# Kernel optimization log

Hardware: AMD Instinct MI355X
Metric: run time of the kernel (lower is better)

Reference implementation:

```python
import jax, jax.numpy as jnp
import numpy as np
from jax import lax

D_MODEL = 1024
D_INNER = 2 * D_MODEL          # expand=2
D_STATE = 16
D_CONV = 4
DT_RANK = 64                   # ceil(1024/16)
DT_MIN = 0.001
DT_MAX = 0.1
BATCH = 4
SEQ = 2048


def setup_inputs() -> dict:
    key = jax.random.key(0)
    ks = jax.random.split(key, 8)
    s = lambda fan_in: 1.0 / np.sqrt(fan_in)
    x = jax.random.normal(ks[0], (BATCH, SEQ, D_MODEL), dtype=jnp.float32)
    # Linear weights stored as (in, out) so y = x @ W
    W_in = jax.random.uniform(ks[1], (D_MODEL, 2 * D_INNER), jnp.float32, -s(D_MODEL), s(D_MODEL))
    conv_w = jax.random.uniform(ks[2], (D_INNER, 1, D_CONV), jnp.float32, -s(D_CONV), s(D_CONV))
    conv_b = jax.random.uniform(ks[3], (D_INNER,), jnp.float32, -s(D_CONV), s(D_CONV))
    W_x = jax.random.uniform(ks[4], (D_INNER, DT_RANK + 2 * D_STATE), jnp.float32, -s(D_INNER), s(D_INNER))
    W_dt = jax.random.uniform(ks[5], (DT_RANK, D_INNER), jnp.float32, -s(DT_RANK), s(DT_RANK))
    b_dt = jax.random.uniform(ks[6], (D_INNER,), jnp.float32, -s(DT_RANK), s(DT_RANK))
    # A = arange(1..d_state) repeated over d_inner; store log(A)
    A_log = jnp.log(jnp.broadcast_to(jnp.arange(1, D_STATE + 1, dtype=jnp.float32), (D_INNER, D_STATE)))
    D_param = jnp.ones((D_INNER,), dtype=jnp.float32)
    W_out = jax.random.uniform(ks[7], (D_INNER, D_MODEL), jnp.float32, -s(D_INNER), s(D_INNER))
    return {"x": x, "W_in": W_in, "conv_w": conv_w, "conv_b": conv_b,
            "W_x": W_x, "W_dt": W_dt, "b_dt": b_dt, "A_log": A_log,
            "D_param": D_param, "W_out": W_out}


def reference(x, W_in, conv_w, conv_b, W_x, W_dt, b_dt, A_log, D_param, W_out):
    # in_proj + split
    xz = x @ W_in                                   # (B, S, 2*d_inner)
    x_branch, z_branch = jnp.split(xz, 2, axis=-1)  # each (B, S, d_inner)

    # causal depthwise conv1d (torch pads d_conv-1 both sides then slices [:seq])
    xc = jnp.pad(x_branch.transpose(0, 2, 1), ((0, 0), (0, 0), (D_CONV - 1, 0)))
    xc = lax.conv_general_dilated(xc, conv_w, (1,), 'VALID',
                                  dimension_numbers=('NCH', 'OIH', 'NCH'),
                                  feature_group_count=D_INNER)
    xc = xc + conv_b[None, :, None]
    x_conv = jax.nn.silu(xc.transpose(0, 2, 1))     # (B, S, d_inner)

    # input-dependent dt, B, C
    x_dbl = x_conv @ W_x                            # (B, S, dt_rank + 2*d_state)
    dt_low = x_dbl[..., :DT_RANK]
    Bm = x_dbl[..., DT_RANK:DT_RANK + D_STATE]      # (B, S, d_state)
    Cm = x_dbl[..., DT_RANK + D_STATE:]             # (B, S, d_state)
    dt = jax.nn.sigmoid(dt_low @ W_dt + b_dt) * (DT_MAX - DT_MIN) + DT_MIN
    dt = jnp.maximum(dt, 1e-4)                      # (B, S, d_inner)

    A = -jnp.exp(A_log)                             # (d_inner, d_state)

    # selective scan over time (n_substeps = 1)
    def step(h, inp):
        dt_t, B_t, C_t, x_t = inp                   # (B,di), (B,ds), (B,ds), (B,di)
        dA = jnp.exp(dt_t[:, :, None] * A[None])    # (B, di, ds)
        h = dA * h + (dt_t * x_t)[:, :, None] * B_t[:, None, :]
        y_t = jnp.sum(h * C_t[:, None, :], axis=-1) # (B, di)
        return h, y_t

    h0 = jnp.zeros((x.shape[0], D_INNER, D_STATE), dtype=x.dtype)
    _, ys = lax.scan(step, h0,
                     (dt.swapaxes(0, 1), Bm.swapaxes(0, 1),
                      Cm.swapaxes(0, 1), x_conv.swapaxes(0, 1)))
    y = ys.swapaxes(0, 1)                           # (B, S, d_inner)

    y = y + x_conv * D_param
    y = y * jax.nn.silu(z_branch)
    return y @ W_out                                # (B, S, d_model)
```

## Files before the change

kernel.cpp:

```cpp
#include <hip/hip_runtime.h>

typedef unsigned short u16;
typedef unsigned int u32;
typedef __attribute__((ext_vector_type(8))) short short8;
typedef __attribute__((ext_vector_type(4))) short short4v;
typedef __attribute__((ext_vector_type(2))) short short2v;
typedef __attribute__((ext_vector_type(4))) float f32x4;

#define NBATCH 4
#define NSEQ   2048
#define DMODEL 1024
#define DINNER 2048
#define DSTATE 16
#define DTRANK 64
#define ROWS   (NBATCH*NSEQ)
#define NCH    64
#define CLEN   32

__device__ __forceinline__ float b2f(u16 u){ union{u32 i; float f;} v; v.i=((u32)u)<<16; return v.f; }
__device__ __forceinline__ u16 f2b(float f){ union{float f; u32 i;} v; v.f=f; u32 i=v.i; return (u16)((i + 0x7FFFu + ((i>>16)&1u))>>16); }
__device__ __forceinline__ float sigmoidf_(float x){ return 1.0f/(1.0f+__expf(-x)); }

__device__ __forceinline__ void pow16(float e1, float (&pw)[16]){
  float p2 = e1*e1, p4 = p2*p2, p8 = p4*p4;
  pw[0]=e1;        pw[1]=p2;        pw[2]=e1*p2;     pw[3]=p4;
  pw[4]=e1*p4;     pw[5]=p2*p4;     pw[6]=pw[2]*p4;  pw[7]=p8;
  pw[8]=e1*p8;     pw[9]=p2*p8;     pw[10]=pw[2]*p8; pw[11]=p4*p8;
  pw[12]=pw[4]*p8; pw[13]=pw[5]*p8; pw[14]=pw[6]*p8; pw[15]=p8*p8;
}

__global__ __launch_bounds__(256) void prep(const u16* __restrict__ x,
    const u16* __restrict__ Win, const u16* __restrict__ convw,
    const u16* __restrict__ Wx, const u16* __restrict__ Wdt,
    const u16* __restrict__ Alog, const u16* __restrict__ Wout,
    const u16* __restrict__ v0, const u16* __restrict__ v1, const u16* __restrict__ v2,
    int* __restrict__ meta){
  __shared__ int vote;
  __shared__ int mxbits;
  const int tid = threadIdx.x;
  const u16* V[3] = {v0, v1, v2};

  const u16* ptrs[6] = {x, Win, convw, Wx, Wdt, Wout};
  const float bounds[6] = {8.f, 0.045f, 0.6f, 0.035f, 0.15f, 0.035f};
  const int slots[6] = {0, 1, 2, 4, 5, 9};
  for (int q = 0; q < 6; q++){
    if (tid == 0) vote = 1;
    __syncthreads();
    int bad = 0;
    for (int i = tid; i < 2048; i += 256){
      float v = fabsf(b2f(ptrs[q][i]));
      if (!(v <= bounds[q])) bad = 1;
    }
    if (bad) atomicAnd(&vote, 0);
    __syncthreads();
    if (tid == 0) meta[slots[q]] = vote;
    __syncthreads();
  }
  if (tid == 0){ u16 u = Alog[1]; meta[7] = (u == 0x3F31 || u == 0x3F32) ? 1 : 0; }

  int iD = -1, fD = 1;
  for (int k = 0; k < 3; k++){
    if (V[k][0] == 0x3F80 && V[k][1] == 0x3F80){ iD = k; fD = 1; }
    else if (V[k][0] == 0 && V[k][1] == 0x3F80 && V[k][2] == 0){ iD = k; fD = 0; }
  }
  if (iD < 0){ iD = 2; fD = 1; }
  int oo[2], no = 0;
  for (int k = 0; k < 3; k++) if (k != iD) oo[no++] = k;
  int fo[2]; float mo[2];
  for (int q = 0; q < 2; q++){
    if (tid == 0) vote = 1;
    __syncthreads();
    int bad = 0;
    for (int i = tid; i < 2048; i += 256){
      float v = fabsf(b2f(V[oo[q]][i]));
      if (!(v <= 0.6f)) bad = 1;
    }
    if (bad) atomicAnd(&vote, 0);
    __syncthreads();
    fo[q] = vote;
    if (tid == 0) mxbits = 0;
    __syncthreads();
    float m = 0.f;
    for (int i = tid; i < 2048; i += 256){
      float v = fabsf(fo[q] ? b2f(V[oo[q]][i]) : ((const float*)V[oo[q]])[i]);
      m = fmaxf(m, v);
    }
    atomicMax(&mxbits, __float_as_int(m));
    __syncthreads();
    mo[q] = __int_as_float(mxbits);
    __syncthreads();
  }
  if (tid == 0){
    int a = (mo[0] > 0.25f) ? 0 : 1;
    meta[10] = oo[a];     meta[3] = fo[a];
    meta[11] = oo[1-a];   meta[6] = fo[1-a];
    meta[12] = iD;        meta[8] = fD;
  }
}

__global__ __launch_bounds__(256) void cvt_bf16(const void* __restrict__ in,
                                                u16* __restrict__ out, long n,
                                                const int* __restrict__ meta, int slot){
  long i = (long)blockIdx.x*256 + threadIdx.x;
  if (i >= n) return;
  if (meta[slot]) out[i] = ((const u16*)in)[i];
  else            out[i] = f2b(((const float*)in)[i]);
}

__global__ __launch_bounds__(256) void cvt_x8(const void* __restrict__ in,
                                              u16* __restrict__ out,
                                              const int* __restrict__ meta){
  long i8 = ((long)blockIdx.x*256 + threadIdx.x)*8;
  if (meta[0]){
    *(short8*)(out + i8) = *(const short8*)((const u16*)in + i8);
  } else {
    const float* f = (const float*)in + i8;
    f32x4 a = *(const f32x4*)f;
    f32x4 b = *(const f32x4*)(f+4);
    short8 o;
    #pragma unroll
    for (int j=0;j<4;j++){ ((u16*)&o)[j] = f2b(a[j]); ((u16*)&o)[4+j] = f2b(b[j]); }
    *(short8*)(out + i8) = o;
  }
}

__global__ __launch_bounds__(256) void cvt_trio(const void* __restrict__ v0,
                                                const void* __restrict__ v1,
                                                const void* __restrict__ v2,
                                                const int* __restrict__ meta,
                                                u16* __restrict__ cbc,
                                                u16* __restrict__ bdtc,
                                                u16* __restrict__ dpc){
  int i = blockIdx.x*256 + threadIdx.x;
  int which = i >> 11, d = i & 2047;
  const void* V[3] = {v0, v1, v2};
  int src, fl; u16* dst;
  if (which == 0){ src = meta[10]; fl = meta[3]; dst = cbc; }
  else if (which == 1){ src = meta[11]; fl = meta[6]; dst = bdtc; }
  else { src = meta[12]; fl = meta[8]; dst = dpc; }
  dst[d] = fl ? ((const u16*)V[src])[d] : f2b(((const float*)V[src])[d]);
}

__global__ __launch_bounds__(256) void transpose_pad(const void* __restrict__ inv,
                                                     u16* __restrict__ out,
                                                     int K, int N, int Nout,
                                                     const int* __restrict__ meta, int slot){
  __shared__ u16 t[32][33];
  const int f = meta[slot];
  const u16*   ib = (const u16*)inv;
  const float* iff = (const float*)inv;
  int k0 = blockIdx.x*32, n0 = blockIdx.y*32;
  int tx = threadIdx.x & 31, ty = threadIdx.x >> 5;
  #pragma unroll
  for (int i=0;i<32;i+=8){
    int k = k0+ty+i, n = n0+tx;
    u16 v = 0;
    if (k<K && n<N) v = f ? ib[(long)k*N+n] : f2b(iff[(long)k*N+n]);
    t[ty+i][tx] = v;
  }
  __syncthreads();
  #pragma unroll
  for (int i=0;i<32;i+=8){
    int n = n0+ty+i, k = k0+tx;
    if (n<Nout && k<K) out[(long)n*K+k] = t[tx][ty+i];
  }
}

template<int MODE>
__global__ __launch_bounds__(256) void gemm_bt(
    const u16* __restrict__ A, int lda,
    const u16* __restrict__ Bt, int K,
    u16* __restrict__ C0, u16* __restrict__ C1, int ldc,
    const u16* __restrict__ bias, float* __restrict__ Cf)
{
  __shared__ u16 sa[128*64];
  __shared__ u16 sb[128*64];
  const int tid = threadIdx.x;
  const int lane = tid & 63;
  const int wave = tid >> 6;
  const int wm = (wave >> 1) * 64;
  const int wn = (wave & 1) * 64;
  const int lane15 = lane & 15;
  const int quad = lane >> 4;
  const long rowBase = (long)blockIdx.y * 128;
  const long colBase = (long)blockIdx.x * 128;

  int kbeg = 0, kend = K;
  if (MODE == 4){
    const int span = K >> 2;
    kbeg = blockIdx.z * span;
    kend = kbeg + span;
    Cf += (long)blockIdx.z * (8192L*128);
  }

  f32x4 acc[4][4];
  #pragma unroll
  for (int i=0;i<4;i++)
    #pragma unroll
    for (int j=0;j<4;j++)
      #pragma unroll
      for (int r=0;r<4;r++) acc[i][j][r]=0.0f;

  const int e  = tid*8;
  const int r0 = e >> 6;
  const int c0 = e & 63;

  for (int kb=kbeg; kb<kend; kb+=64) {
    #pragma unroll
    for (int i=0;i<4;i++){
      const u16* ga = A + (rowBase + r0 + i*32)*lda + kb + c0;
      __builtin_amdgcn_global_load_lds((const __attribute__((address_space(1))) void*)ga,
                                       (__attribute__((address_space(3))) void*)&sa[e + i*2048],
                                       16, 0, 0);
    }
    #pragma unroll
    for (int i=0;i<4;i++){
      const u16* gb = Bt + (colBase + r0 + i*32)*(long)K + kb + c0;
      __builtin_amdgcn_global_load_lds((const __attribute__((address_space(1))) void*)gb,
                                       (__attribute__((address_space(3))) void*)&sb[e + i*2048],
                                       16, 0, 0);
    }
    __syncthreads();
    #pragma unroll
    for (int ko=0; ko<2; ko++){
      const int kk = ko*32 + quad*8;
      short8 af[4], bfr[4];
      #pragma unroll
      for (int i=0;i<4;i++) af[i]  = *(const short8*)&sa[(wm + i*16 + lane15)*64 + kk];
      #pragma unroll
      for (int j=0;j<4;j++) bfr[j] = *(const short8*)&sb[(wn + j*16 + lane15)*64 + kk];
      #pragma unroll
      for (int i=0;i<4;i++)
        #pragma unroll
        for (int j=0;j<4;j++)
          acc[i][j] = __builtin_amdgcn_mfma_f32_16x16x32_bf16(af[i], bfr[j], acc[i][j], 0, 0, 0);
    }
    __syncthreads();
  }

  #pragma unroll
  for (int i=0;i<4;i++){
    #pragma unroll
    for (int j=0;j<4;j++){
      long row = rowBase + wm + i*16 + quad*4;
      long col = colBase + wn + j*16 + lane15;
      #pragma unroll
      for (int r=0;r<4;r++){
        float v = acc[i][j][r];
        long rr = row + r;
        if (MODE == 0) {
          C0[rr*ldc + col] = f2b(v);
        } else if (MODE == 2) {
          float t  = sigmoidf_(v + b2f(bias[col]));
          float dv = fmaxf(t*0.099f + 0.001f, 1e-4f);
          C0[rr*ldc + col] = f2b(dv);
        } else if (MODE == 4) {
          Cf[rr*ldc + col] = v;
        }
      }
    }
  }
}

__global__ __launch_bounds__(256) void reduce_xdbl(const float* __restrict__ P,
                                                   u16* __restrict__ out){
  const long i4 = ((long)blockIdx.x*256 + threadIdx.x)*4;
  f32x4 a = *(const f32x4*)(P + i4);
  f32x4 b = *(const f32x4*)(P + 1048576 + i4);
  f32x4 c = *(const f32x4*)(P + 2097152 + i4);
  f32x4 d = *(const f32x4*)(P + 3145728 + i4);
  short4v o;
  #pragma unroll
  for (int j=0;j<4;j++) ((u16*)&o)[j] = f2b(a[j]+b[j]+c[j]+d[j]);
  *(short4v*)(out + i4) = o;
}

template<int MODE>
__global__ __launch_bounds__(512, 2) void gemm256(
    const u16* __restrict__ A, int lda,
    const u16* __restrict__ Bt, int K,
    u16* __restrict__ C0, u16* __restrict__ C1, int ldc,
    float* __restrict__ Cf)
{
  __shared__ u16 sa[2*16384];
  __shared__ u16 sb[2*16384];
  const int tid  = threadIdx.x;
  const int lane = tid & 63;
  const int wm   = (tid >> 6) >> 2;
  const int wn   = (tid >> 6) & 3;
  const int lane15 = lane & 15;
  const int quad   = lane >> 4;

  const int nwg  = gridDim.x * gridDim.y;
  const int orig = blockIdx.y * gridDim.x + blockIdx.x;
  const int swz  = (orig & 7) * (nwg >> 3) + (orig >> 3);
  const int bx   = swz % gridDim.x;
  const int by   = swz / gridDim.x;
  const long rowBase = (long)by * 256;
  const long colBase = (long)bx * 256;

  const int xorv = (lane15 & 7) << 3;
  const int k0   = (quad*8) ^ xorv;
  const int k1   = (32 + quad*8) ^ xorv;
  const int aBase = (wm*128 + lane15) * 64;
  const int bBase = (wn*64  + lane15) * 64;

  const int scol = ((tid & 7) ^ ((tid >> 3) & 7)) << 3;
  const int arow = tid >> 3;
  const int bsub = ((tid >> 8) & 1)*64 + ((tid & 255) >> 3);
  const int bdst = (tid & 7) * 8;

  f32x4 acc[8][4];
  #pragma unroll
  for (int i=0;i<8;i++)
    #pragma unroll
    for (int j=0;j<4;j++)
      #pragma unroll
      for (int r=0;r<4;r++) acc[i][j][r]=0.0f;

  const int nt = K >> 6;

  auto stageA = [&](int buf, int rs, int kb){
    const u16* g = A + (rowBase + rs + arow)*(long)lda + kb + scol;
    __builtin_amdgcn_global_load_lds((const __attribute__((address_space(1))) void*)g,
        (__attribute__((address_space(3))) void*)&sa[buf*16384 + rs*64 + tid*8], 16, 0, 0);
  };
  auto stageB = [&](int buf, int cq, int part, int kb){
    const int row = part*128 + cq*32 + bsub;
    const u16* g = Bt + (colBase + row)*(long)K + kb + scol;
    __builtin_amdgcn_global_load_lds((const __attribute__((address_space(1))) void*)g,
        (__attribute__((address_space(3))) void*)&sb[buf*16384 + row*64 + bdst], 16, 0, 0);
  };

  stageA(0,   0, 0); stageA(0, 128, 0);
  stageB(0, 0, 0, 0); stageB(0, 0, 1, 0);
  stageA(0,  64, 0); stageA(0, 192, 0);
  stageB(0, 1, 0, 0); stageB(0, 1, 1, 0);
  asm volatile("s_waitcnt vmcnt(4)\n\ts_barrier" ::: "memory");

  for (int t = 0; t < nt; ++t){
    const int cur = t & 1, nb = cur ^ 1;
    const int kb2 = (t+1) << 6;
    const bool pf = (t+1 < nt);
    const u16* sA = &sa[cur*16384];
    const u16* sB = &sb[cur*16384];
    short8 a0[4][2], a1[4][2], b0[2][2], b1[2][2];

    #pragma unroll
    for (int i=0;i<4;i++){
      a0[i][0] = *(const short8*)&sA[aBase + i*1024 + k0];
      a0[i][1] = *(const short8*)&sA[aBase + i*1024 + k1];
    }
    #pragma unroll
    for (int j=0;j<2;j++){
      b0[j][0] = *(const short8*)&sB[bBase + j*1024 + k0];
      b0[j][1] = *(const short8*)&sB[bBase + j*1024 + k1];
    }
    if (pf){ stageA(nb, 0, kb2); stageA(nb, 128, kb2); }
    __builtin_amdgcn_s_setprio(1);
    #pragma unroll
    for (int s=0;s<2;s++)
      #pragma unroll
      for (int i=0;i<4;i++)
        #pragma unroll
        for (int j=0;j<2;j++)
          acc[i][j] = __builtin_amdgcn_mfma_f32_16x16x32_bf16(a0[i][s], b0[j][s], acc[i][j], 0, 0, 0);
    __builtin_amdgcn_s_setprio(0);
    asm volatile("s_waitcnt vmcnt(4)\n\ts_barrier" ::: "memory");

    #pragma unroll
    for (int i=0;i<4;i++){
      a1[i][0] = *(const short8*)&sA[aBase + 4096 + i*1024 + k0];
      a1[i][1] = *(const short8*)&sA[aBase + 4096 + i*1024 + k1];
    }
    if (pf){ stageB(nb, 0, 0, kb2); stageB(nb, 0, 1, kb2); }
    __builtin_amdgcn_s_setprio(1);
    #pragma unroll
    for (int s=0;s<2;s++)
      #pragma unroll
      for (int i=0;i<4;i++)
        #pragma unroll
        for (int j=0;j<2;j++)
          acc[4+i][j] = __builtin_amdgcn_mfma_f32_16x16x32_bf16(a1[i][s], b0[j][s], acc[4+i][j], 0, 0, 0);
    __builtin_amdgcn_s_setprio(0);
    asm volatile("s_waitcnt vmcnt(4)\n\ts_barrier" ::: "memory");

    #pragma unroll
    for (int j=0;j<2;j++){
      b1[j][0] = *(const short8*)&sB[bBase + 2048 + j*1024 + k0];
      b1[j][1] = *(const short8*)&sB[bBase + 2048 + j*1024 + k1];
    }
    if (pf){ stageA(nb, 64, kb2); stageA(nb, 192, kb2); }
    __builtin_amdgcn_s_setprio(1);
    #pragma unroll
    for (int s=0;s<2;s++)
      #pragma unroll
      for (int i=0;i<4;i++)
        #pragma unroll
        for (int j=0;j<2;j++)
          acc[i][2+j] = __builtin_amdgcn_mfma_f32_16x16x32_bf16(a0[i][s], b1[j][s], acc[i][2+j], 0, 0, 0);
    __builtin_amdgcn_s_setprio(0);
    asm volatile("s_barrier" ::: "memory");

    if (pf){ stageB(nb, 1, 0, kb2); stageB(nb, 1, 1, kb2); }
    __builtin_amdgcn_s_setprio(1);
    #pragma unroll
    for (int s=0;s<2;s++)
      #pragma unroll
      for (int i=0;i<4;i++)
        #pragma unroll
        for (int j=0;j<2;j++)
          acc[4+i][2+j] = __builtin_amdgcn_mfma_f32_16x16x32_bf16(a1[i][s], b1[j][s], acc[4+i][2+j], 0, 0, 0);
    __builtin_amdgcn_s_setprio(0);
    asm volatile("s_waitcnt vmcnt(4)\n\ts_barrier" ::: "memory");
  }

  #pragma unroll
  for (int i=0;i<8;i++){
    const long row = rowBase + wm*128 + i*16 + quad*4;
    #pragma unroll
    for (int j=0;j<4;j++){
      const long col = colBase + wn*64 + j*16 + lane15;
      #pragma unroll
      for (int r=0;r<4;r++){
        const float v = acc[i][j][r];
        const long rr = row + r;
        if (MODE == 1){
          if (col < 2048) C0[rr*2048 + col] = f2b(v);
          else            C1[rr*2048 + (col-2048)] = f2b(v);
        } else {
          Cf[rr*ldc + col] = v;
        }
      }
    }
  }
}

__global__ __launch_bounds__(512, 2) void gemm_out(
    const u16* __restrict__ A, int lda,
    const u16* __restrict__ Bt, int K,
    float* __restrict__ Cf, int ldc)
{
  __shared__ u16 sa[2*16384];
  __shared__ u16 sb[2*8192];
  const int tid  = threadIdx.x;
  const int lane = tid & 63;
  const int wm   = (tid >> 6) >> 2;
  const int wn   = (tid >> 6) & 3;
  const int lane15 = lane & 15;
  const int quad   = lane >> 4;

  const int nwg  = gridDim.x * gridDim.y;
  const int orig = blockIdx.y * gridDim.x + blockIdx.x;
  const int swz  = (orig & 7) * (nwg >> 3) + (orig >> 3);
  const int bx   = swz % gridDim.x;
  const int by   = swz / gridDim.x;
  const long rowBase = (long)by * 256;
  const long colBase = (long)bx * 128;

  const int xorv = (lane15 & 7) << 3;
  const int k0   = (quad*8) ^ xorv;
  const int k1   = (32 + quad*8) ^ xorv;
  const int aBase = (wm*128 + lane15) * 64;
  const int bBase = (wn*32  + lane15) * 64;

  const int scol = ((tid & 7) ^ ((tid >> 3) & 7)) << 3;
  const int arow = tid >> 3;

  f32x4 acc[8][2];
  #pragma unroll
  for (int i=0;i<8;i++)
    #pragma unroll
    for (int j=0;j<2;j++)
      #pragma unroll
      for (int r=0;r<4;r++) acc[i][j][r]=0.0f;

  const int nt = K >> 6;

  auto stageA = [&](int buf, int rs, int kb){
    const u16* g = A + (rowBase + rs + arow)*(long)lda + kb + scol;
    __builtin_amdgcn_global_load_lds((const __attribute__((address_space(1))) void*)g,
        (__attribute__((address_space(3))) void*)&sa[buf*16384 + rs*64 + tid*8], 16, 0, 0);
  };
  auto stageB = [&](int buf, int rs, int kb){
    const u16* g = Bt + (colBase + rs + arow)*(long)K + kb + scol;
    __builtin_amdgcn_global_load_lds((const __attribute__((address_space(1))) void*)g,
        (__attribute__((address_space(3))) void*)&sb[buf*8192 + rs*64 + tid*8], 16, 0, 0);
  };

  stageA(0,0,0); stageA(0,128,0); stageB(0,0,0); stageB(0,64,0);
  stageA(0,64,0); stageA(0,192,0);
  asm volatile("s_waitcnt vmcnt(0)\n\ts_barrier" ::: "memory");

  for (int t = 0; t < nt; ++t){
    const int cur = t & 1, nb = cur ^ 1;
    const int kb2 = (t+1) << 6;
    const bool pf = (t+1 < nt);
    const u16* sA = &sa[cur*16384];
    const u16* sB = &sb[cur*8192];
    short8 a0[4][2], a1[4][2], bf_[2][2];

    #pragma unroll
    for (int i=0;i<4;i++){
      a0[i][0] = *(const short8*)&sA[aBase + i*1024 + k0];
      a0[i][1] = *(const short8*)&sA[aBase + i*1024 + k1];
    }
    #pragma unroll
    for (int j=0;j<2;j++){
      bf_[j][0] = *(const short8*)&sB[bBase + j*1024 + k0];
      bf_[j][1] = *(const short8*)&sB[bBase + j*1024 + k1];
    }
    if (pf){ stageA(nb,0,kb2); stageA(nb,128,kb2); stageB(nb,0,kb2); stageB(nb,64,kb2); }
    __builtin_amdgcn_s_setprio(1);
    #pragma unroll
    for (int s=0;s<2;s++)
      #pragma unroll
      for (int i=0;i<4;i++)
        #pragma unroll
        for (int j=0;j<2;j++)
          acc[i][j] = __builtin_amdgcn_mfma_f32_16x16x32_bf16(a0[i][s], bf_[j][s], acc[i][j], 0, 0, 0);
    __builtin_amdgcn_s_setprio(0);
    asm volatile("s_waitcnt vmcnt(4)\n\ts_barrier" ::: "memory");

    #pragma unroll
    for (int i=0;i<4;i++){
      a1[i][0] = *(const short8*)&sA[aBase + 4096 + i*1024 + k0];
      a1[i][1] = *(const short8*)&sA[aBase + 4096 + i*1024 + k1];
    }
    if (pf){ stageA(nb,64,kb2); stageA(nb,192,kb2); }
    __builtin_amdgcn_s_setprio(1);
    #pragma unroll
    for (int s=0;s<2;s++)
      #pragma unroll
      for (int i=0;i<4;i++)
        #pragma unroll
        for (int j=0;j<2;j++)
          acc[4+i][j] = __builtin_amdgcn_mfma_f32_16x16x32_bf16(a1[i][s], bf_[j][s], acc[4+i][j], 0, 0, 0);
    __builtin_amdgcn_s_setprio(0);
    asm volatile("s_waitcnt vmcnt(2)\n\ts_barrier" ::: "memory");
  }

  #pragma unroll
  for (int i=0;i<8;i++){
    const long row = rowBase + wm*128 + i*16 + quad*4;
    #pragma unroll
    for (int j=0;j<2;j++){
      const long col = colBase + wn*32 + j*16 + lane15;
      #pragma unroll
      for (int r=0;r<4;r++)
        Cf[(row + r)*ldc + col] = acc[i][j][r];
    }
  }
}

__global__ __launch_bounds__(256) void conv_silu4(const u16* __restrict__ xb,
                                                  const u16* __restrict__ w,
                                                  const u16* __restrict__ bias,
                                                  u16* __restrict__ xc){
  const int idx = blockIdx.x*256 + threadIdx.x;
  const int dg = idx & 255;
  const int sg = (idx >> 8) & 511;
  const int b  = idx >> 17;
  const int d  = dg*8;
  const int s0 = sg*4;

  short8 bv = *(const short8*)(bias + d);
  short8 wv0 = *(const short8*)(w + d*4);
  short8 wv1 = *(const short8*)(w + d*4 + 8);
  short8 wv2 = *(const short8*)(w + d*4 + 16);
  short8 wv3 = *(const short8*)(w + d*4 + 24);
  u16 wl[32];
  #pragma unroll
  for (int q=0;q<8;q++){ wl[q] = ((u16*)&wv0)[q]; wl[8+q] = ((u16*)&wv1)[q];
                         wl[16+q] = ((u16*)&wv2)[q]; wl[24+q] = ((u16*)&wv3)[q]; }

  short8 xr[7];
  #pragma unroll
  for (int q=0;q<7;q++){
    int t = s0 - 3 + q;
    short8 z;
    #pragma unroll
    for (int l=0;l<8;l++) ((u16*)&z)[l] = 0;
    if (t >= 0) z = *(const short8*)(xb + ((long)(b*NSEQ + t))*DINNER + d);
    xr[q] = z;
  }

  #pragma unroll
  for (int st=0; st<4; st++){
    float acc[8];
    #pragma unroll
    for (int l=0;l<8;l++) acc[l] = b2f(((u16*)&bv)[l]);
    #pragma unroll
    for (int j=0;j<4;j++){
      const short8& xv = xr[st + j];
      #pragma unroll
      for (int l=0;l<8;l++)
        acc[l] += b2f(((u16*)&xv)[l]) * b2f(wl[l*4 + j]);
    }
    short8 ov;
    #pragma unroll
    for (int l=0;l<8;l++){ float y = acc[l]*sigmoidf_(acc[l]); ((u16*)&ov)[l] = f2b(y); }
    *(short8*)(xc + ((long)(b*NSEQ + s0 + st))*DINNER + d) = ov;
  }
}

__global__ __launch_bounds__(256) void scan_pass1(const u16* __restrict__ dt,
                                                  const u16* __restrict__ xc,
                                                  const u16* __restrict__ xdbl,
                                                  const u16* __restrict__ Alog,
                                                  float* __restrict__ hend,
                                                  float* __restrict__ sumdt){
  const int tid = threadIdx.x;
  const int d0 = blockIdx.x*512 + tid*2;
  const int c = blockIdx.y;
  const int b = blockIdx.z;
  __shared__ float sB[CLEN][DSTATE];
  for (int i=tid; i<CLEN*DSTATE; i+=256){
    int t = i >> 4, s = i & 15;
    sB[t][s] = b2f(xdbl[((long)(b*NSEQ + c*CLEN + t))*128 + DTRANK + s]);
  }
  bool fast = true;
  #pragma unroll
  for (int j=0;j<2;j++)
    #pragma unroll
    for (int s=0;s<DSTATE;s++){
      float a = -__expf(b2f(Alog[(d0+j)*DSTATE + s]));
      fast = fast && (fabsf(a + (float)(s+1)) < 0.03f*(float)(s+1));
    }
  __syncthreads();

  float h[2][DSTATE];
  #pragma unroll
  for (int j=0;j<2;j++)
    #pragma unroll
    for (int s=0;s<DSTATE;s++) h[j][s] = 0.0f;
  float sd[2] = {0.f,0.f};
  long base = ((long)(b*NSEQ + c*CLEN))*DINNER + d0;
  short2v dt2 = *(const short2v*)(dt + base);
  short2v x2  = *(const short2v*)(xc + base);
  if (fast){
    for (int t=0;t<CLEN;t++){
      long nxt = base + (long)((t+1<CLEN)?(t+1):t)*DINNER;
      short2v dtn = *(const short2v*)(dt + nxt);
      short2v xn  = *(const short2v*)(xc + nxt);
      float B[DSTATE];
      *(f32x4*)&B[0]  = *(const f32x4*)&sB[t][0];
      *(f32x4*)&B[4]  = *(const f32x4*)&sB[t][4];
      *(f32x4*)&B[8]  = *(const f32x4*)&sB[t][8];
      *(f32x4*)&B[12] = *(const f32x4*)&sB[t][12];
      #pragma unroll
      for (int j=0;j<2;j++){
        float dtv = b2f(((u16*)&dt2)[j]);
        float xv  = b2f(((u16*)&x2)[j]);
        float u = dtv*xv;
        sd[j] += dtv;
        float e1 = __expf(-dtv);
        float pw[16];
        pow16(e1, pw);
        #pragma unroll
        for (int s=0;s<DSTATE;s++)
          h[j][s] = fmaf(pw[s], h[j][s], u*B[s]);
      }
      dt2 = dtn; x2 = xn;
    }
  } else {
    float Acf[2][DSTATE];
    #pragma unroll
    for (int j=0;j<2;j++)
      #pragma unroll
      for (int s=0;s<DSTATE;s++) Acf[j][s] = -__expf(b2f(Alog[(d0+j)*DSTATE + s]));
    for (int t=0;t<CLEN;t++){
      long nxt = base + (long)((t+1<CLEN)?(t+1):t)*DINNER;
      short2v dtn = *(const short2v*)(dt + nxt);
      short2v xn  = *(const short2v*)(xc + nxt);
      float B[DSTATE];
      *(f32x4*)&B[0]  = *(const f32x4*)&sB[t][0];
      *(f32x4*)&B[4]  = *(const f32x4*)&sB[t][4];
      *(f32x4*)&B[8]  = *(const f32x4*)&sB[t][8];
      *(f32x4*)&B[12] = *(const f32x4*)&sB[t][12];
      #pragma unroll
      for (int j=0;j<2;j++){
        float dtv = b2f(((u16*)&dt2)[j]);
        float xv  = b2f(((u16*)&x2)[j]);
        float u = dtv*xv;
        sd[j] += dtv;
        #pragma unroll
        for (int s=0;s<DSTATE;s++){
          float dA = __expf(dtv * Acf[j][s]);
          h[j][s] = fmaf(dA, h[j][s], u*B[s]);
        }
      }
      dt2 = dtn; x2 = xn;
    }
  }
  #pragma unroll
  for (int j=0;j<2;j++){
    long hidx = ((long)(b*DINNER + d0 + j)*NCH + c)*DSTATE;
    #pragma unroll
    for (int q=0;q<4;q++) *(f32x4*)&hend[hidx + q*4] = *(const f32x4*)&h[j][q*4];
    sumdt[(long)(b*DINNER + d0 + j)*NCH + c] = sd[j];
  }
}

__global__ __launch_bounds__(256) void scan_pass2(float* __restrict__ hend,
                                                  const float* __restrict__ sumdt,
                                                  const u16* __restrict__ Alog){
  long i = (long)blockIdx.x*256 + threadIdx.x;
  int s = (int)(i & 15);
  long bd = i >> 4;
  int d = (int)(bd & (DINNER-1));
  float A = -__expf(b2f(Alog[d*DSTATE + s]));
  float run = 0.0f;
  long base = bd*NCH*DSTATE + s;
  for (int c=0;c<NCH;c++){
    float e = hend[base + (long)c*DSTATE];
    float decay = __expf(A * sumdt[bd*NCH + c]);
    hend[base + (long)c*DSTATE] = run;
    run = run*decay + e;
  }
}

__global__ __launch_bounds__(256) void scan_pass3(const u16* __restrict__ dt,
                                                  u16* __restrict__ xc,
                                                  const u16* __restrict__ zb,
                                                  const u16* __restrict__ xdbl,
                                                  const u16* __restrict__ Alog,
                                                  const u16* __restrict__ Dp,
                                                  const float* __restrict__ hstart){
  const int tid = threadIdx.x;
  const int d0 = blockIdx.x*512 + tid*2;
  const int c = blockIdx.y;
  const int b = blockIdx.z;
  __shared__ float sB[CLEN][DSTATE];
  __shared__ float sC[CLEN][DSTATE];
  for (int i=tid; i<CLEN*DSTATE; i+=256){
    int t = i >> 4, s = i & 15;
    long rb = ((long)(b*NSEQ + c*CLEN + t))*128;
    sB[t][s] = b2f(xdbl[rb + DTRANK + s]);
    sC[t][s] = b2f(xdbl[rb + DTRANK + DSTATE + s]);
  }
  bool fast = true;
  #pragma unroll
  for (int j=0;j<2;j++)
    #pragma unroll
    for (int s=0;s<DSTATE;s++){
      float a = -__expf(b2f(Alog[(d0+j)*DSTATE + s]));
      fast = fast && (fabsf(a + (float)(s+1)) < 0.03f*(float)(s+1));
    }
  __syncthreads();

  float h[2][DSTATE];
  #pragma unroll
  for (int j=0;j<2;j++){
    long hidx = ((long)(b*DINNER + d0 + j)*NCH + c)*DSTATE;
    #pragma unroll
    for (int q=0;q<4;q++) *(f32x4*)&h[j][q*4] = *(const f32x4*)&hstart[hidx + q*4];
  }
  short2v dp2 = *(const short2v*)(Dp + d0);
  long base = ((long)(b*NSEQ + c*CLEN))*DINNER + d0;
  short2v dt2 = *(const short2v*)(dt + base);
  short2v x2  = *(const short2v*)(xc + base);
  short2v z2  = *(const short2v*)(zb + base);
  if (fast){
    for (int t=0;t<CLEN;t++){
      long nxt = base + (long)((t+1<CLEN)?(t+1):t)*DINNER;
      short2v dtn = *(const short2v*)(dt + nxt);
      short2v xn  = *(const short2v*)(xc + nxt);
      short2v zn  = *(const short2v*)(zb + nxt);
      float B[DSTATE], C[DSTATE];
      *(f32x4*)&B[0]  = *(const f32x4*)&sB[t][0];
      *(f32x4*)&B[4]  = *(const f32x4*)&sB[t][4];
      *(f32x4*)&B[8]  = *(const f32x4*)&sB[t][8];
      *(f32x4*)&B[12] = *(const f32x4*)&sB[t][12];
      *(f32x4*)&C[0]  = *(const f32x4*)&sC[t][0];
      *(f32x4*)&C[4]  = *(const f32x4*)&sC[t][4];
      *(f32x4*)&C[8]  = *(const f32x4*)&sC[t][8];
      *(f32x4*)&C[12] = *(const f32x4*)&sC[t][12];
      short2v ov;
      #pragma unroll
      for (int j=0;j<2;j++){
        float dtv = b2f(((u16*)&dt2)[j]);
        float xv  = b2f(((u16*)&x2)[j]);
        float zv  = b2f(((u16*)&z2)[j]);
        float u = dtv*xv;
        float e1 = __expf(-dtv);
        float gate = zv*sigmoidf_(zv);
        float pw[16];
        pow16(e1, pw);
        float y0=0.f, y1=0.f, y2=0.f, y3=0.f;
        #pragma unroll
        for (int q=0;q<4;q++){
          h[j][q*4+0] = fmaf(pw[q*4+0], h[j][q*4+0], u*B[q*4+0]);
          h[j][q*4+1] = fmaf(pw[q*4+1], h[j][q*4+1], u*B[q*4+1]);
          h[j][q*4+2] = fmaf(pw[q*4+2], h[j][q*4+2], u*B[q*4+2]);
          h[j][q*4+3] = fmaf(pw[q*4+3], h[j][q*4+3], u*B[q*4+3]);
          y0 = fmaf(h[j][q*4+0], C[q*4+0], y0);
          y1 = fmaf(h[j][q*4+1], C[q*4+1], y1);
          y2 = fmaf(h[j][q*4+2], C[q*4+2], y2);
          y3 = fmaf(h[j][q*4+3], C[q*4+3], y3);
        }
        float y = (y0+y1)+(y2+y3);
        y = fmaf(xv, b2f(((u16*)&dp2)[j]), y);
        y *= gate;
        ((u16*)&ov)[j] = f2b(y);
      }
      *(short2v*)(xc + base + (long)t*DINNER) = ov;
      dt2 = dtn; x2 = xn; z2 = zn;
    }
  } else {
    float Acf[2][DSTATE];
    #pragma unroll
    for (int j=0;j<2;j++)
      #pragma unroll
      for (int s=0;s<DSTATE;s++) Acf[j][s] = -__expf(b2f(Alog[(d0+j)*DSTATE + s]));
    for (int t=0;t<CLEN;t++){
      long nxt = base + (long)((t+1<CLEN)?(t+1):t)*DINNER;
      short2v dtn = *(const short2v*)(dt + nxt);
      short2v xn  = *(const short2v*)(xc + nxt);
      short2v zn  = *(const short2v*)(zb + nxt);
      float B[DSTATE], C[DSTATE];
      *(f32x4*)&B[0]  = *(const f32x4*)&sB[t][0];
      *(f32x4*)&B[4]  = *(const f32x4*)&sB[t][4];
      *(f32x4*)&B[8]  = *(const f32x4*)&sB[t][8];
      *(f32x4*)&B[12] = *(const f32x4*)&sB[t][12];
      *(f32x4*)&C[0]  = *(const f32x4*)&sC[t][0];
      *(f32x4*)&C[4]  = *(const f32x4*)&sC[t][4];
      *(f32x4*)&C[8]  = *(const f32x4*)&sC[t][8];
      *(f32x4*)&C[12] = *(const f32x4*)&sC[t][12];
      short2v ov;
      #pragma unroll
      for (int j=0;j<2;j++){
        float dtv = b2f(((u16*)&dt2)[j]);
        float xv  = b2f(((u16*)&x2)[j]);
        float zv  = b2f(((u16*)&z2)[j]);
        float u = dtv*xv;
        float gate = zv*sigmoidf_(zv);
        float y = 0.0f;
        #pragma unroll
        for (int s=0;s<DSTATE;s++){
          float dA = __expf(dtv * Acf[j][s]);
          h[j][s] = fmaf(dA, h[j][s], u*B[s]);
          y = fmaf(h[j][s], C[s], y);
        }
        y = fmaf(xv, b2f(((u16*)&dp2)[j]), y);
        y *= gate;
        ((u16*)&ov)[j] = f2b(y);
      }
      *(short2v*)(xc + base + (long)t*DINNER) = ov;
      dt2 = dtn; x2 = xn; z2 = zn;
    }
  }
}

extern "C" void kernel_launch(void* const* d_in, const int* in_sizes, int n_in,
                              void* d_out, int out_size, void* d_ws, size_t ws_size,
                              hipStream_t stream) {
  const void *x=nullptr,*W_in=nullptr,*conv_w=nullptr,*W_x=nullptr,*W_dt=nullptr,
             *A_log=nullptr,*W_out=nullptr;
  const void* v2048[3] = {nullptr,nullptr,nullptr};
  int n2048 = 0;
  for (int i = 0; i < n_in; i++){
    switch (in_sizes[i]){
      case 8388608: x      = d_in[i]; break;
      case 4194304: W_in   = d_in[i]; break;
      case 8192:    conv_w = d_in[i]; break;
      case 196608:  W_x    = d_in[i]; break;
      case 131072:  W_dt   = d_in[i]; break;
      case 32768:   A_log  = d_in[i]; break;
      case 2097152: W_out  = d_in[i]; break;
      case 2048:    if (n2048 < 3) v2048[n2048++] = d_in[i]; break;
      default: break;
    }
  }

  size_t off = 0;
  char* wsb = (char*)d_ws;
  auto take = [&](size_t n){ void* p = wsb + off; off += (n + 255) & ~(size_t)255; return p; };
  u16* Wt_in  = (u16*)take((size_t)4096*1024*2);
  u16* Wt_x   = (u16*)take((size_t)128*2048*2);
  u16* Wt_dt  = (u16*)take((size_t)2048*64*2);
  u16* Wt_out = (u16*)take((size_t)1024*2048*2);
  u16* xb     = (u16*)take((size_t)ROWS*DINNER*2);
  u16* zb     = (u16*)take((size_t)ROWS*DINNER*2);
  u16* xc     = (u16*)take((size_t)ROWS*DINNER*2);
  u16* xdbl   = (u16*)take((size_t)ROWS*128*2);
  char* shr = (char*)take((size_t)ROWS*NCH*DSTATE*4 + (size_t)ROWS*NCH*4 + 4096);
  u16*   xcvt  = (u16*)shr;
  float* hend  = (float*)shr;
  float* sumdt = (float*)(shr + (size_t)ROWS*NCH*DSTATE*4);
  u16* cwc  = (u16*)take(DINNER*4*2);
  u16* cbc  = (u16*)take(DINNER*2);
  u16* bdtc = (u16*)take(DINNER*2);
  u16* alc  = (u16*)take(DINNER*DSTATE*2);
  u16* dpc  = (u16*)take(DINNER*2);
  int* meta = (int*)take(256);
  float* xdp = (float*)take((size_t)4*8192*128*4);
  u16* dtb = xb;

  prep<<<1, 256, 0, stream>>>((const u16*)x, (const u16*)W_in, (const u16*)conv_w,
                              (const u16*)W_x, (const u16*)W_dt, (const u16*)A_log,
                              (const u16*)W_out,
                              (const u16*)v2048[0], (const u16*)v2048[1], (const u16*)v2048[2],
                              meta);

  cvt_x8<<<(ROWS*DMODEL)/(256*8), 256, 0, stream>>>(x, xcvt, meta);
  cvt_bf16<<<32, 256, 0, stream>>>(conv_w, cwc, DINNER*4, meta, 2);
  cvt_bf16<<<128,256, 0, stream>>>(A_log, alc, DINNER*DSTATE, meta, 7);
  cvt_trio<<<24, 256, 0, stream>>>(v2048[0], v2048[1], v2048[2], meta, cbc, bdtc, dpc);

  transpose_pad<<<dim3(32,128), 256, 0, stream>>>(W_in, Wt_in, 1024, 4096, 4096, meta, 1);
  transpose_pad<<<dim3(64,4),   256, 0, stream>>>(W_x,  Wt_x,  2048, 96,   128,  meta, 4);
  transpose_pad<<<dim3(2,64),   256, 0, stream>>>(W_dt, Wt_dt, 64,   2048, 2048, meta, 5);
  transpose_pad<<<dim3(64,32),  256, 0, stream>>>(W_out,Wt_out,2048, 1024, 1024, meta, 9);

  gemm256<1><<<dim3(16,32), 512, 0, stream>>>(xcvt, 1024, Wt_in, 1024, xb, zb, 2048, nullptr);

  conv_silu4<<<(ROWS*DINNER)/(256*32), 256, 0, stream>>>(xb, cwc, cbc, xc);

  gemm_bt<4><<<dim3(1,64,4), 256, 0, stream>>>(xc, 2048, Wt_x, 2048, nullptr, nullptr, 128, nullptr, xdp);
  reduce_xdbl<<<1024, 256, 0, stream>>>(xdp, xdbl);

  gemm_bt<2><<<dim3(16,64), 256, 0, stream>>>(xdbl, 128, Wt_dt, 64, dtb, nullptr, 2048, bdtc, nullptr);

  scan_pass1<<<dim3(4,NCH,NBATCH), 256, 0, stream>>>(dtb, xc, xdbl, alc, hend, sumdt);
  scan_pass2<<<(ROWS*DSTATE)/256, 256, 0, stream>>>(hend, sumdt, alc);
  scan_pass3<<<dim3(4,NCH,NBATCH), 256, 0, stream>>>(dtb, xc, zb, xdbl, alc, dpc, hend);

  gemm_out<<<dim3(8,32), 512, 0, stream>>>(xc, 2048, Wt_out, 2048, (float*)d_out, 1024);
}
```

Baseline: 444.6 us.

## Parallelize chunk-carry scan with wavefront shuffle scan and merge small conversion kernels

The inter-chunk state propagation pass now gives each (batch, channel, state) series a full 64-lane wavefront and runs a Hillis-Steele associative scan over the 64 chunks with shuffles. Before, a single thread walked all chunks in sequence. This replaces a serial 64-step dependency chain with log-depth work, at the cost of far more threads and redundant multiplies. Separately, three small parameter-conversion launches are merged into one kernel to cut launch overhead.

After: 483.7 us. 1.09x slower.

```diff
diff --git a/kernel.cpp b/kernel.cpp
--- a/kernel.cpp
+++ b/kernel.cpp
@@ -98,15 +98,6 @@
   }
 }
 
-__global__ __launch_bounds__(256) void cvt_bf16(const void* __restrict__ in,
-                                                u16* __restrict__ out, long n,
-                                                const int* __restrict__ meta, int slot){
-  long i = (long)blockIdx.x*256 + threadIdx.x;
-  if (i >= n) return;
-  if (meta[slot]) out[i] = ((const u16*)in)[i];
-  else            out[i] = f2b(((const float*)in)[i]);
-}
-
 __global__ __launch_bounds__(256) void cvt_x8(const void* __restrict__ in,
                                               u16* __restrict__ out,
                                               const int* __restrict__ meta){
@@ -124,21 +115,33 @@
   }
 }
 
-__global__ __launch_bounds__(256) void cvt_trio(const void* __restrict__ v0,
-                                                const void* __restrict__ v1,
-                                                const void* __restrict__ v2,
-                                                const int* __restrict__ meta,
-                                                u16* __restrict__ cbc,
-                                                u16* __restrict__ bdtc,
-                                                u16* __restrict__ dpc){
+__global__ __launch_bounds__(256) void cvt_small(const void* __restrict__ convw,
+                                                 const void* __restrict__ Alog,
+                                                 const void* __restrict__ v0,
+                                                 const void* __restrict__ v1,
+                                                 const void* __restrict__ v2,
+                                                 const int* __restrict__ meta,
+                                                 u16* __restrict__ cwc,
+                                                 u16* __restrict__ alc,
+                                                 u16* __restrict__ cbc,
+                                                 u16* __restrict__ bdtc,
+                                                 u16* __restrict__ dpc){
   int i = blockIdx.x*256 + threadIdx.x;
-  int which = i >> 11, d = i & 2047;
-  const void* V[3] = {v0, v1, v2};
-  int src, fl; u16* dst;
-  if (which == 0){ src = meta[10]; fl = meta[3]; dst = cbc; }
-  else if (which == 1){ src = meta[11]; fl = meta[6]; dst = bdtc; }
-  else { src = meta[12]; fl = meta[8]; dst = dpc; }
-  dst[d] = fl ? ((const u16*)V[src])[d] : f2b(((const float*)V[src])[d]);
+  if (i < 8192){
+    cwc[i] = meta[2] ? ((const u16*)convw)[i] : f2b(((const float*)convw)[i]);
+  } else if (i < 40960){
+    int k = i - 8192;
+    alc[k] = meta[7] ? ((const u16*)Alog)[k] : f2b(((const float*)Alog)[k]);
+  } else if (i < 47104){
+    int k = i - 40960;
+    int which = k >> 11, d = k & 2047;
+    const void* V[3] = {v0, v1, v2};
+    int src, fl; u16* dst;
+    if (which == 0){ src = meta[10]; fl = meta[3]; dst = cbc; }
+    else if (which == 1){ src = meta[11]; fl = meta[6]; dst = bdtc; }
+    else { src = meta[12]; fl = meta[8]; dst = dpc; }
+    dst[d] = fl ? ((const u16*)V[src])[d] : f2b(((const float*)V[src])[d]);
+  }
 }
 
 __global__ __launch_bounds__(256) void transpose_pad(const void* __restrict__ inv,
@@ -702,22 +705,31 @@
   }
 }
 
-__global__ __launch_bounds__(256) void scan_pass2(float* __restrict__ hend,
-                                                  const float* __restrict__ sumdt,
-                                                  const u16* __restrict__ Alog){
-  long i = (long)blockIdx.x*256 + threadIdx.x;
-  int s = (int)(i & 15);
-  long bd = i >> 4;
-  int d = (int)(bd & (DINNER-1));
-  float A = -__expf(b2f(Alog[d*DSTATE + s]));
-  float run = 0.0f;
-  long base = bd*NCH*DSTATE + s;
-  for (int c=0;c<NCH;c++){
-    float e = hend[base + (long)c*DSTATE];
-    float decay = __expf(A * sumdt[bd*NCH + c]);
-    hend[base + (long)c*DSTATE] = run;
-    run = run*decay + e;
-  }
+__global__ __launch_bounds__(256) void scan_pass2p(float* __restrict__ hend,
+                                                   const float* __restrict__ sumdt,
+                                                   const u16* __restrict__ Alog){
+  const long gw = ((long)blockIdx.x*256 + threadIdx.x) >> 6;
+  const int lane = threadIdx.x & 63;
+  const int s = (int)(gw & 15);
+  const long bd = gw >> 4;
+  const int d = (int)(bd & (DINNER-1));
+  const float A = -__expf(b2f(Alog[d*DSTATE + s]));
+  const long base = bd*NCH*DSTATE + s;
+
+  float e = hend[base + (long)lane*DSTATE];
+  float a = __expf(A * sumdt[bd*NCH + lane]);
+  #pragma unroll
+  for (int off=1; off<64; off<<=1){
+    float a_up = __shfl_up(a, off);
+    float e_up = __shfl_up(e, off);
+    if (lane >= off){
+      e = fmaf(e_up, a, e);
+      a *= a_up;
+    }
+  }
+  float e_ex = __shfl_up(e, 1);
+  if (lane == 0) e_ex = 0.0f;
+  hend[base + (long)lane*DSTATE] = e_ex;
 }
 
 __global__ __launch_bounds__(256) void scan_pass3(const u16* __restrict__ dt,
@@ -904,9 +916,8 @@
                               meta);
 
   cvt_x8<<<(ROWS*DMODEL)/(256*8), 256, 0, stream>>>(x, xcvt, meta);
-  cvt_bf16<<<32, 256, 0, stream>>>(conv_w, cwc, DINNER*4, meta, 2);
-  cvt_bf16<<<128,256, 0, stream>>>(A_log, alc, DINNER*DSTATE, meta, 7);
-  cvt_trio<<<24, 256, 0, stream>>>(v2048[0], v2048[1], v2048[2], meta, cbc, bdtc, dpc);
+  cvt_small<<<184, 256, 0, stream>>>(conv_w, A_log, v2048[0], v2048[1], v2048[2],
+                                     meta, cwc, alc, cbc, bdtc, dpc);
 
   transpose_pad<<<dim3(32,128), 256, 0, stream>>>(W_in, Wt_in, 1024, 4096, 4096, meta, 1);
   transpose_pad<<<dim3(64,4),   256, 0, stream>>>(W_x,  Wt_x,  2048, 96,   128,  meta, 4);
@@ -923,7 +934,7 @@
   gemm_bt<2><<<dim3(16,64), 256, 0, stream>>>(xdbl, 128, Wt_dt, 64, dtb, nullptr, 2048, bdtc, nullptr);
 
   scan_pass1<<<dim3(4,NCH,NBATCH), 256, 0, stream>>>(dtb, xc, xdbl, alc, hend, sumdt);
-  scan_pass2<<<(ROWS*DSTATE)/256, 256, 0, stream>>>(hend, sumdt, alc);
+  scan_pass2p<<<32768, 256, 0, stream>>>(hend, sumdt, alc);
   scan_pass3<<<dim3(4,NCH,NBATCH), 256, 0, stream>>>(dtb, xc, zb, xdbl, alc, dpc, hend);
 
   gemm_out<<<dim3(8,32), 512, 0, stream>>>(xc, 2048, Wt_out, 2048, (float*)d_out, 1024);
```
